# Optimization experiments

Measured on AMD Instinct MI355X. Metric: run time of the kernel, lower is better.

The kernel has to match this reference:

```python
import jax, jax.numpy as jnp
import numpy as np

U, H = 1024, 4096  # num_users, hidden_size; d_inner = 2*H = 8192


def setup_inputs() -> dict:
    key = jax.random.key(0)
    k0, k1, k2, k3 = jax.random.split(key, 4)
    x = jax.random.normal(k0, (U, H), dtype=jnp.float32)
    ssm_proj = jax.random.uniform(k1, (H, 2 * H), dtype=jnp.float32)  # torch.rand init
    conv_states = jnp.zeros((4, U, 2 * H), dtype=jnp.float32)          # ttnn.zeros init
    conv_wts = jax.random.uniform(k2, (4, 2 * H), dtype=jnp.float32)   # 4 taps, per-channel
    conv_bias = jax.random.uniform(k3, (2 * H,), dtype=jnp.float32)
    return {"x": x, "ssm_proj": ssm_proj, "conv_states": conv_states,
            "conv_wts": conv_wts, "conv_bias": conv_bias}


def reference(x, ssm_proj, conv_states, conv_wts, conv_bias):
    # in-projection: [U,H] @ [H,2H] -> [U,2H]
    xp = x @ ssm_proj
    # shift the 4-tap causal-conv state cache and append current step
    new_states = jnp.concatenate([conv_states[1:], xp[None]], axis=0)  # [4,U,2H]
    # depthwise 4-tap causal conv as weighted sum over taps + bias
    out = jnp.einsum("kd,kud->ud", conv_wts, new_states) + conv_bias   # [U,2H]
    # (downstream TtMambaSSM consumes `out`; external class, not part of this block's math)
    return out, new_states
```

## Files before the change

kernel.cpp:

```cpp
#include <hip/hip_runtime.h>
#include <hip/hip_bf16.h>

#define U_DIM 1024
#define H_DIM 4096
#define N_DIM 8192
#define K_DIM 4096

#define BM 128
#define BN 256
#define BK 64
#define NT (K_DIM / BK)
#define SLOTB (BM*BK*2 + BN*BK*2)

typedef __attribute__((ext_vector_type(8))) short bf16x8;
typedef __attribute__((ext_vector_type(4))) float f32x4;

__device__ inline unsigned short f2bf(float f) {
  union { float f; unsigned u; } a; a.f = f;
  unsigned r = a.u + 0x7fffu + ((a.u >> 16) & 1u);
  return (unsigned short)(r >> 16);
}

__device__ inline void gload_lds16(const void* g, void* l) {
  __builtin_amdgcn_global_load_lds(
      (const __attribute__((address_space(1))) unsigned*)(g),
      (__attribute__((address_space(3))) unsigned*)(l), 16, 0, 0);
}

#define TRANS_BLOCKS ((N_DIM / 64) * (K_DIM / 64))
__global__ __launch_bounds__(256) void prep_kernel(
    const float* __restrict__ B, unsigned short* __restrict__ Bt,
    const float* __restrict__ x, unsigned short* __restrict__ xb) {
  const int tid = threadIdx.x;
  if (blockIdx.x >= TRANS_BLOCKS) {
    size_t i = (size_t)(blockIdx.x - TRANS_BLOCKS) * 256 + tid;
    float4 v = ((const float4*)x)[i];
    ushort4 o;
    o.x = f2bf(v.x); o.y = f2bf(v.y); o.z = f2bf(v.z); o.w = f2bf(v.w);
    ((ushort4*)xb)[i] = o;
    return;
  }
  __shared__ float tile[64][65];
  const int kt = blockIdx.x & 63;
  const int nt = blockIdx.x >> 6;
  const int k0 = kt * 64, n0 = nt * 64;
  const int lr = tid >> 4;
  const int lc = (tid & 15) * 4;
#pragma unroll
  for (int it = 0; it < 4; ++it) {
    int r = it * 16 + lr;
    float4 v = *(const float4*)(&B[(size_t)(k0 + r) * N_DIM + n0 + lc]);
    tile[r][lc + 0] = v.x; tile[r][lc + 1] = v.y;
    tile[r][lc + 2] = v.z; tile[r][lc + 3] = v.w;
  }
  __syncthreads();
  const int sc = tid & 7;
  const int sr = tid >> 3;
#pragma unroll
  for (int it = 0; it < 2; ++it) {
    int rn = it * 32 + sr;
    union { bf16x8 v; unsigned short u[8]; } o;
#pragma unroll
    for (int j = 0; j < 8; ++j) o.u[j] = f2bf(tile[sc * 8 + j][rn]);
    *(bf16x8*)(&Bt[(size_t)(n0 + rn) * K_DIM + k0 + sc * 8]) = o.v;
  }
}

template <bool FUSE>
__global__ __launch_bounds__(512, 1) void gemm_conv_kernel(
    const unsigned short* __restrict__ Abf,
    const unsigned short* __restrict__ Btbf,
    const float* __restrict__ conv_states,
    const float* __restrict__ conv_wts,
    const float* __restrict__ conv_bias,
    float* __restrict__ out,
    float* __restrict__ ns)
{
  __shared__ char smem[3 * SLOTB];

  const int orig = blockIdx.x;
  const int bid  = (orig & 7) * 32 + (orig >> 3);
  const int brow = bid & 7;
  const int bcol = bid >> 3;
  const int tid  = threadIdx.x;
  const int lane = tid & 63;
  const int wid  = tid >> 6;
  const int wr = wid >> 2;
  const int wc = wid & 3;

  f32x4 acc[4][4];
#pragma unroll
  for (int m = 0; m < 4; ++m)
#pragma unroll
    for (int n = 0; n < 4; ++n)
#pragma unroll
      for (int r = 0; r < 4; ++r) acc[m][n][r] = 0.0f;

  const int rowa = tid >> 3;
  const int gsl  = (tid & 7) ^ (rowa & 7);
  const int tid16 = tid * 16;
  const unsigned short* gA0 = Abf  + (size_t)(brow * BM + rowa) * K_DIM + gsl * 8;
  const unsigned short* gA1 = gA0 + (size_t)64 * K_DIM;
  const unsigned short* gB0 = Btbf + (size_t)(bcol * BN + rowa) * K_DIM + gsl * 8;
  const unsigned short* gB1 = gB0 + (size_t)64  * K_DIM;
  const unsigned short* gB2 = gB0 + (size_t)128 * K_DIM;
  const unsigned short* gB3 = gB0 + (size_t)192 * K_DIM;

#define STAGE(kt, base) do {                               \
    const size_t ko = (size_t)(kt) * BK;                   \
    gload_lds16(gA0 + ko, (base) + tid16);                 \
    gload_lds16(gA1 + ko, (base) + 8192  + tid16);         \
    gload_lds16(gB0 + ko, (base) + 16384 + tid16);         \
    gload_lds16(gB1 + ko, (base) + 24576 + tid16);         \
    gload_lds16(gB2 + ko, (base) + 32768 + tid16);         \
    gload_lds16(gB3 + ko, (base) + 40960 + tid16);         \
  } while (0)

  const int l15 = lane & 15;
  const int fs  = lane >> 4;
  const int rsw = l15 & 7;
  int aoff[4], boff[4];
#pragma unroll
  for (int m = 0; m < 4; ++m) aoff[m] = (wr * 64 + m * 16 + l15) * 128;
#pragma unroll
  for (int n = 0; n < 4; ++n) boff[n] = (wc * 64 + n * 16 + l15) * 128;

  STAGE(0, smem);
  STAGE(1, smem + SLOTB);
  asm volatile("s_waitcnt vmcnt(6)" ::: "memory");
  __builtin_amdgcn_s_barrier();
  __builtin_amdgcn_sched_barrier(0);

  int s0 = 0, s2 = 2;
#pragma unroll 1
  for (int t = 0; t < NT; ++t) {
    if (t + 2 < NT) STAGE(t + 2, smem + s2 * SLOTB);

    const char* curA = smem + s0 * SLOTB;
    const char* curB = curA + 16384;
#pragma unroll
    for (int kh = 0; kh < 2; ++kh) {
      const int ksl = ((kh * 4 + fs) ^ rsw) * 16;
      bf16x8 af[4], bv[4];
#pragma unroll
      for (int m = 0; m < 4; ++m) af[m] = *(const bf16x8*)(curA + aoff[m] + ksl);
#pragma unroll
      for (int n = 0; n < 4; ++n) bv[n] = *(const bf16x8*)(curB + boff[n] + ksl);
      __builtin_amdgcn_s_setprio(1);
#pragma unroll
      for (int m = 0; m < 4; ++m)
#pragma unroll
        for (int n = 0; n < 4; ++n)
          acc[m][n] = __builtin_amdgcn_mfma_f32_16x16x32_bf16(af[m], bv[n], acc[m][n], 0, 0, 0);
      __builtin_amdgcn_s_setprio(0);
    }

    if (t + 2 < NT) asm volatile("s_waitcnt vmcnt(6) lgkmcnt(0)" ::: "memory");
    else            asm volatile("s_waitcnt vmcnt(0) lgkmcnt(0)" ::: "memory");
    __builtin_amdgcn_s_barrier();
    __builtin_amdgcn_sched_barrier(0);

    s0 = (s0 == 2) ? 0 : s0 + 1;
    s2 = (s2 == 2) ? 0 : s2 + 1;
  }
#undef STAGE

  float* cbuf = (float*)smem;
#pragma unroll
  for (int m = 0; m < 4; ++m)
#pragma unroll
    for (int n = 0; n < 4; ++n) {
      const int colb = (wc * 64 + n * 16 + l15) ^ (fs << 3);
#pragma unroll
      for (int r = 0; r < 4; ++r) {
        const int row = wr * 64 + m * 16 + fs * 4 + r;
        cbuf[row * 256 + colb] = acc[m][n][r];
      }
    }
  __syncthreads();

  const size_t PL4 = (size_t)U_DIM * (N_DIM / 4);
  const float4* cs1 = (const float4*)conv_states + PL4;
  const float4* cs2 = (const float4*)conv_states + 2 * PL4;
  const float4* cs3 = (const float4*)conv_states + 3 * PL4;
  float4* out4 = (float4*)out;
  float4* ns0 = (float4*)ns;
  float4* ns1 = ns0 + PL4;
  float4* ns2 = ns0 + 2 * PL4;
  float4* ns3 = ns0 + 3 * PL4;
  const float4* wt4 = (const float4*)conv_wts;
  const float4* bi4 = (const float4*)conv_bias;

#pragma unroll 1
  for (int i = 0; i < 16; ++i) {
    const int g    = i * 512 + tid;
    const int lrow = g >> 6;
    const int d4   = g & 63;
    const int fsr  = (lrow >> 2) & 3;
    const float4 xp4 = *(const float4*)&cbuf[lrow * 256 + ((d4 * 4) ^ (fsr << 3))];

    const int u = brow * BM + lrow;
    const int dcol4 = bcol * (BN / 4) + d4;
    const size_t gf4 = (size_t)u * (N_DIM / 4) + dcol4;

    const float4 w0 = wt4[dcol4];
    const float4 w1 = wt4[(N_DIM / 4) + dcol4];
    const float4 w2 = wt4[2 * (N_DIM / 4) + dcol4];
    const float4 w3 = wt4[3 * (N_DIM / 4) + dcol4];
    const float4 bs = bi4[dcol4];
    const float4 c1 = cs1[gf4];
    const float4 c2 = cs2[gf4];
    const float4 c3 = cs3[gf4];

    float4 o;
    o.x = fmaf(w0.x, c1.x, fmaf(w1.x, c2.x, fmaf(w2.x, c3.x, fmaf(w3.x, xp4.x, bs.x))));
    o.y = fmaf(w0.y, c1.y, fmaf(w1.y, c2.y, fmaf(w2.y, c3.y, fmaf(w3.y, xp4.y, bs.y))));
    o.z = fmaf(w0.z, c1.z, fmaf(w1.z, c2.z, fmaf(w2.z, c3.z, fmaf(w3.z, xp4.z, bs.z))));
    o.w = fmaf(w0.w, c1.w, fmaf(w1.w, c2.w, fmaf(w2.w, c3.w, fmaf(w3.w, xp4.w, bs.w))));

    out4[gf4] = o;
    if (FUSE) { ns0[gf4] = c1; ns1[gf4] = c2; ns2[gf4] = c3; }
    ns3[gf4] = xp4;
  }
}

extern "C" void kernel_launch(void* const* d_in, const int* in_sizes, int n_in,
                              void* d_out, int out_size, void* d_ws, size_t ws_size,
                              hipStream_t stream) {
  (void)in_sizes; (void)n_in; (void)out_size;
  const float* x           = (const float*)d_in[0];
  const float* ssm_proj    = (const float*)d_in[1];
  const float* conv_states = (const float*)d_in[2];
  const float* conv_wts    = (const float*)d_in[3];
  const float* conv_bias   = (const float*)d_in[4];
  float* outp = (float*)d_out;

  const size_t OUT_ELEMS = (size_t)U_DIM * N_DIM;
  float* ns = outp + OUT_ELEMS;

  const size_t BT_BYTES = (size_t)N_DIM * K_DIM * sizeof(unsigned short);
  const size_t XB_BYTES = (size_t)U_DIM * K_DIM * sizeof(unsigned short);
  const int GRID = (U_DIM / BM) * (N_DIM / BN);
  const int PREP_GRID = TRANS_BLOCKS + (U_DIM * H_DIM / 4) / 256;

  if (ws_size >= BT_BYTES + XB_BYTES) {
    unsigned short* Btbf = (unsigned short*)d_ws;
    unsigned short* xbf  = (unsigned short*)((char*)d_ws + BT_BYTES);
    prep_kernel<<<PREP_GRID, 256, 0, stream>>>(ssm_proj, Btbf, x, xbf);
    gemm_conv_kernel<true><<<GRID, 512, 0, stream>>>(
        xbf, Btbf, conv_states, conv_wts, conv_bias, outp, ns);
  } else {
    unsigned short* Btbf = (unsigned short*)ns;
    unsigned short* xbf  = (unsigned short*)(ns + 2 * OUT_ELEMS);
    prep_kernel<<<PREP_GRID, 256, 0, stream>>>(ssm_proj, Btbf, x, xbf);
    gemm_conv_kernel<false><<<GRID, 512, 0, stream>>>(
        xbf, Btbf, conv_states, conv_wts, conv_bias, outp, ns);
    hipMemcpyAsync(ns, conv_states + OUT_ELEMS, 3 * OUT_ELEMS * sizeof(float),
                   hipMemcpyDeviceToDevice, stream);
  }
}
```

Baseline: 170.4 us.

## Shrink GEMM tiles to 128x128x32 and allow multiple blocks per CU

Reduces the block tile from 128x256 with BK 64 to 128x128 with BK 32. The per-thread staging, swizzle pattern, fragment offsets and epilogue indexing are rewritten to match the smaller tile. The launch bound now permits several resident blocks per CU, and the grid doubles to 512 blocks. The aim is better occupancy and CU load balance, so more waves hide memory latency. In exchange, each block gets less operand reuse, does fewer MFMAs per barrier, and the total global/L2 traffic for the B and A operands grows.

```diff
diff --git a/kernel.cpp b/kernel.cpp
--- a/kernel.cpp
+++ b/kernel.cpp
@@ -7,8 +7,8 @@
 #define K_DIM 4096
 
 #define BM 128
-#define BN 256
-#define BK 64
+#define BN 128
+#define BK 32
 #define NT (K_DIM / BK)
 #define SLOTB (BM*BK*2 + BN*BK*2)
 
@@ -67,7 +67,7 @@
 }
 
 template <bool FUSE>
-__global__ __launch_bounds__(512, 1) void gemm_conv_kernel(
+__global__ __launch_bounds__(512, 4) void gemm_conv_kernel(
     const unsigned short* __restrict__ Abf,
     const unsigned short* __restrict__ Btbf,
     const float* __restrict__ conv_states,
@@ -76,10 +76,10 @@
     float* __restrict__ out,
     float* __restrict__ ns)
 {
-  __shared__ char smem[3 * SLOTB];
+  __shared__ char smem[65536];
 
   const int orig = blockIdx.x;
-  const int bid  = (orig & 7) * 32 + (orig >> 3);
+  const int bid  = (orig & 7) * 64 + (orig >> 3);
   const int brow = bid & 7;
   const int bcol = bid >> 3;
   const int tid  = threadIdx.x;
@@ -88,46 +88,38 @@
   const int wr = wid >> 2;
   const int wc = wid & 3;
 
-  f32x4 acc[4][4];
+  f32x4 acc[4][2];
 #pragma unroll
   for (int m = 0; m < 4; ++m)
 #pragma unroll
-    for (int n = 0; n < 4; ++n)
+    for (int n = 0; n < 2; ++n)
 #pragma unroll
       for (int r = 0; r < 4; ++r) acc[m][n][r] = 0.0f;
 
-  const int rowa = tid >> 3;
-  const int gsl  = (tid & 7) ^ (rowa & 7);
-  const int tid16 = tid * 16;
-  const unsigned short* gA0 = Abf  + (size_t)(brow * BM + rowa) * K_DIM + gsl * 8;
-  const unsigned short* gA1 = gA0 + (size_t)64 * K_DIM;
-  const unsigned short* gB0 = Btbf + (size_t)(bcol * BN + rowa) * K_DIM + gsl * 8;
-  const unsigned short* gB1 = gB0 + (size_t)64  * K_DIM;
-  const unsigned short* gB2 = gB0 + (size_t)128 * K_DIM;
-  const unsigned short* gB3 = gB0 + (size_t)192 * K_DIM;
+  const int srow   = tid >> 2;
+  const int swslot = (tid & 3) ^ ((srow >> 1) & 3);
+  const int tid16  = tid * 16;
+  const unsigned short* gA0 = Abf  + (size_t)(brow * BM + srow) * K_DIM + swslot * 8;
+  const unsigned short* gB0 = Btbf + (size_t)(bcol * BN + srow) * K_DIM + swslot * 8;
 
 #define STAGE(kt, base) do {                               \
     const size_t ko = (size_t)(kt) * BK;                   \
     gload_lds16(gA0 + ko, (base) + tid16);                 \
-    gload_lds16(gA1 + ko, (base) + 8192  + tid16);         \
-    gload_lds16(gB0 + ko, (base) + 16384 + tid16);         \
-    gload_lds16(gB1 + ko, (base) + 24576 + tid16);         \
-    gload_lds16(gB2 + ko, (base) + 32768 + tid16);         \
-    gload_lds16(gB3 + ko, (base) + 40960 + tid16);         \
+    gload_lds16(gB0 + ko, (base) + 8192 + tid16);          \
   } while (0)
 
   const int l15 = lane & 15;
   const int fs  = lane >> 4;
-  const int rsw = l15 & 7;
-  int aoff[4], boff[4];
-#pragma unroll
-  for (int m = 0; m < 4; ++m) aoff[m] = (wr * 64 + m * 16 + l15) * 128;
-#pragma unroll
-  for (int n = 0; n < 4; ++n) boff[n] = (wc * 64 + n * 16 + l15) * 128;
+  const int rds = (fs ^ ((l15 >> 1) & 3)) * 16;
+  int aoff[4], boff[2];
+#pragma unroll
+  for (int m = 0; m < 4; ++m) aoff[m] = (wr * 64 + m * 16 + l15) * 64 + rds;
+#pragma unroll
+  for (int n = 0; n < 2; ++n) boff[n] = (wc * 32 + n * 16 + l15) * 64 + rds;
 
   STAGE(0, smem);
   STAGE(1, smem + SLOTB);
-  asm volatile("s_waitcnt vmcnt(6)" ::: "memory");
+  asm volatile("s_waitcnt vmcnt(2)" ::: "memory");
   __builtin_amdgcn_s_barrier();
   __builtin_amdgcn_sched_barrier(0);
 
@@ -136,27 +128,23 @@
   for (int t = 0; t < NT; ++t) {
     if (t + 2 < NT) STAGE(t + 2, smem + s2 * SLOTB);
 
-    const char* curA = smem + s0 * SLOTB;
-    const char* curB = curA + 16384;
-#pragma unroll
-    for (int kh = 0; kh < 2; ++kh) {
-      const int ksl = ((kh * 4 + fs) ^ rsw) * 16;
-      bf16x8 af[4], bv[4];
-#pragma unroll
-      for (int m = 0; m < 4; ++m) af[m] = *(const bf16x8*)(curA + aoff[m] + ksl);
-#pragma unroll
-      for (int n = 0; n < 4; ++n) bv[n] = *(const bf16x8*)(curB + boff[n] + ksl);
-      __builtin_amdgcn_s_setprio(1);
-#pragma unroll
-      for (int m = 0; m < 4; ++m)
-#pragma unroll
-        for (int n = 0; n < 4; ++n)
-          acc[m][n] = __builtin_amdgcn_mfma_f32_16x16x32_bf16(af[m], bv[n], acc[m][n], 0, 0, 0);
-      __builtin_amdgcn_s_setprio(0);
-    }
-
-    if (t + 2 < NT) asm volatile("s_waitcnt vmcnt(6) lgkmcnt(0)" ::: "memory");
-    else            asm volatile("s_waitcnt vmcnt(0) lgkmcnt(0)" ::: "memory");
+    const char* sA = smem + s0 * SLOTB;
+    const char* sB = sA + 8192;
+    bf16x8 af[4], bv[2];
+#pragma unroll
+    for (int m = 0; m < 4; ++m) af[m] = *(const bf16x8*)(sA + aoff[m]);
+#pragma unroll
+    for (int n = 0; n < 2; ++n) bv[n] = *(const bf16x8*)(sB + boff[n]);
+    __builtin_amdgcn_s_setprio(1);
+#pragma unroll
+    for (int m = 0; m < 4; ++m)
+#pragma unroll
+      for (int n = 0; n < 2; ++n)
+        acc[m][n] = __builtin_amdgcn_mfma_f32_16x16x32_bf16(af[m], bv[n], acc[m][n], 0, 0, 0);
+    __builtin_amdgcn_s_setprio(0);
+
+    if (t + 2 < NT)      asm volatile("s_waitcnt vmcnt(2) lgkmcnt(0)" ::: "memory");
+    else                 asm volatile("s_waitcnt vmcnt(0) lgkmcnt(0)" ::: "memory");
     __builtin_amdgcn_s_barrier();
     __builtin_amdgcn_sched_barrier(0);
 
@@ -169,12 +157,12 @@
 #pragma unroll
   for (int m = 0; m < 4; ++m)
 #pragma unroll
-    for (int n = 0; n < 4; ++n) {
-      const int colb = (wc * 64 + n * 16 + l15) ^ (fs << 3);
+    for (int n = 0; n < 2; ++n) {
+      const int colb = (wc * 32 + n * 16 + l15) ^ (fs << 3);
 #pragma unroll
       for (int r = 0; r < 4; ++r) {
         const int row = wr * 64 + m * 16 + fs * 4 + r;
-        cbuf[row * 256 + colb] = acc[m][n][r];
+        cbuf[row * 128 + colb] = acc[m][n][r];
       }
     }
   __syncthreads();
@@ -192,12 +180,12 @@
   const float4* bi4 = (const float4*)conv_bias;
 
 #pragma unroll 1
-  for (int i = 0; i < 16; ++i) {
+  for (int i = 0; i < 8; ++i) {
     const int g    = i * 512 + tid;
-    const int lrow = g >> 6;
-    const int d4   = g & 63;
+    const int lrow = g >> 5;
+    const int d4   = g & 31;
     const int fsr  = (lrow >> 2) & 3;
-    const float4 xp4 = *(const float4*)&cbuf[lrow * 256 + ((d4 * 4) ^ (fsr << 3))];
+    const float4 xp4 = *(const float4*)&cbuf[lrow * 128 + ((d4 * 4) ^ (fsr << 3))];
 
     const int u = brow * BM + lrow;
     const int dcol4 = bcol * (BN / 4) + d4;
```

Measured after the change: 188.3 us. +10.5%, slower.

## Add producer warps to overlap conv-state streaming with GEMM main loop

Applied to the files above, without the earlier changes.

Adds two extra warps per block (640 threads) that, during the GEMM k-loop, read the three old conv-state planes, compute the partial conv sum with bias, write it to the output, and copy the shifted states. The epilogue then only re-reads the partial output, adds the last-tap contribution from the GEMM result, and writes the new state plane. This hides the memory-bound conv traffic behind MFMA compute, at the cost of an extra read-modify-write of the output and more threads sharing the barrier. The x-to-bf16 conversion also now handles eight elements per thread.

```diff
diff --git a/kernel.cpp b/kernel.cpp
--- a/kernel.cpp
+++ b/kernel.cpp
@@ -28,16 +28,19 @@
 }
 
 #define TRANS_BLOCKS ((N_DIM / 64) * (K_DIM / 64))
+#define CONV_BLOCKS  ((U_DIM * H_DIM) / (256 * 8))
 __global__ __launch_bounds__(256) void prep_kernel(
     const float* __restrict__ B, unsigned short* __restrict__ Bt,
     const float* __restrict__ x, unsigned short* __restrict__ xb) {
   const int tid = threadIdx.x;
   if (blockIdx.x >= TRANS_BLOCKS) {
     size_t i = (size_t)(blockIdx.x - TRANS_BLOCKS) * 256 + tid;
-    float4 v = ((const float4*)x)[i];
-    ushort4 o;
-    o.x = f2bf(v.x); o.y = f2bf(v.y); o.z = f2bf(v.z); o.w = f2bf(v.w);
-    ((ushort4*)xb)[i] = o;
+    float4 v0 = ((const float4*)x)[2 * i];
+    float4 v1 = ((const float4*)x)[2 * i + 1];
+    union { bf16x8 v; unsigned short u[8]; } o;
+    o.u[0] = f2bf(v0.x); o.u[1] = f2bf(v0.y); o.u[2] = f2bf(v0.z); o.u[3] = f2bf(v0.w);
+    o.u[4] = f2bf(v1.x); o.u[5] = f2bf(v1.y); o.u[6] = f2bf(v1.z); o.u[7] = f2bf(v1.w);
+    ((bf16x8*)xb)[i] = o.v;
     return;
   }
   __shared__ float tile[64][65];
@@ -67,7 +70,7 @@
 }
 
 template <bool FUSE>
-__global__ __launch_bounds__(512, 1) void gemm_conv_kernel(
+__global__ __launch_bounds__(640, 1) void gemm_conv_kernel(
     const unsigned short* __restrict__ Abf,
     const unsigned short* __restrict__ Btbf,
     const float* __restrict__ conv_states,
@@ -85,7 +88,8 @@
   const int tid  = threadIdx.x;
   const int lane = tid & 63;
   const int wid  = tid >> 6;
-  const int wr = wid >> 2;
+  const bool is_compute = (wid < 8);
+  const int wr = (wid >> 2) & 1;
   const int wc = wid & 3;
 
   f32x4 acc[4][4];
@@ -96,9 +100,9 @@
 #pragma unroll
       for (int r = 0; r < 4; ++r) acc[m][n][r] = 0.0f;
 
-  const int rowa = tid >> 3;
+  const int rowa = (tid & 511) >> 3;
   const int gsl  = (tid & 7) ^ (rowa & 7);
-  const int tid16 = tid * 16;
+  const int tid16 = (tid & 511) * 16;
   const unsigned short* gA0 = Abf  + (size_t)(brow * BM + rowa) * K_DIM + gsl * 8;
   const unsigned short* gA1 = gA0 + (size_t)64 * K_DIM;
   const unsigned short* gB0 = Btbf + (size_t)(bcol * BN + rowa) * K_DIM + gsl * 8;
@@ -125,61 +129,8 @@
 #pragma unroll
   for (int n = 0; n < 4; ++n) boff[n] = (wc * 64 + n * 16 + l15) * 128;
 
-  STAGE(0, smem);
-  STAGE(1, smem + SLOTB);
-  asm volatile("s_waitcnt vmcnt(6)" ::: "memory");
-  __builtin_amdgcn_s_barrier();
-  __builtin_amdgcn_sched_barrier(0);
-
-  int s0 = 0, s2 = 2;
-#pragma unroll 1
-  for (int t = 0; t < NT; ++t) {
-    if (t + 2 < NT) STAGE(t + 2, smem + s2 * SLOTB);
-
-    const char* curA = smem + s0 * SLOTB;
-    const char* curB = curA + 16384;
-#pragma unroll
-    for (int kh = 0; kh < 2; ++kh) {
-      const int ksl = ((kh * 4 + fs) ^ rsw) * 16;
-      bf16x8 af[4], bv[4];
-#pragma unroll
-      for (int m = 0; m < 4; ++m) af[m] = *(const bf16x8*)(curA + aoff[m] + ksl);
-#pragma unroll
-      for (int n = 0; n < 4; ++n) bv[n] = *(const bf16x8*)(curB + boff[n] + ksl);
-      __builtin_amdgcn_s_setprio(1);
-#pragma unroll
-      for (int m = 0; m < 4; ++m)
-#pragma unroll
-        for (int n = 0; n < 4; ++n)
-          acc[m][n] = __builtin_amdgcn_mfma_f32_16x16x32_bf16(af[m], bv[n], acc[m][n], 0, 0, 0);
-      __builtin_amdgcn_s_setprio(0);
-    }
-
-    if (t + 2 < NT) asm volatile("s_waitcnt vmcnt(6) lgkmcnt(0)" ::: "memory");
-    else            asm volatile("s_waitcnt vmcnt(0) lgkmcnt(0)" ::: "memory");
-    __builtin_amdgcn_s_barrier();
-    __builtin_amdgcn_sched_barrier(0);
-
-    s0 = (s0 == 2) ? 0 : s0 + 1;
-    s2 = (s2 == 2) ? 0 : s2 + 1;
-  }
-#undef STAGE
-
-  float* cbuf = (float*)smem;
-#pragma unroll
-  for (int m = 0; m < 4; ++m)
-#pragma unroll
-    for (int n = 0; n < 4; ++n) {
-      const int colb = (wc * 64 + n * 16 + l15) ^ (fs << 3);
-#pragma unroll
-      for (int r = 0; r < 4; ++r) {
-        const int row = wr * 64 + m * 16 + fs * 4 + r;
-        cbuf[row * 256 + colb] = acc[m][n][r];
-      }
-    }
-  __syncthreads();
-
   const size_t PL4 = (size_t)U_DIM * (N_DIM / 4);
+  const int    N4  = N_DIM / 4;
   const float4* cs1 = (const float4*)conv_states + PL4;
   const float4* cs2 = (const float4*)conv_states + 2 * PL4;
   const float4* cs3 = (const float4*)conv_states + 3 * PL4;
@@ -191,36 +142,103 @@
   const float4* wt4 = (const float4*)conv_wts;
   const float4* bi4 = (const float4*)conv_bias;
 
+  if (is_compute) {
+    STAGE(0, smem);
+    STAGE(1, smem + SLOTB);
+    asm volatile("s_waitcnt vmcnt(6)" ::: "memory");
+  }
+  __builtin_amdgcn_s_barrier();
+  __builtin_amdgcn_sched_barrier(0);
+
+  int s0 = 0, s2 = 2;
 #pragma unroll 1
-  for (int i = 0; i < 16; ++i) {
-    const int g    = i * 512 + tid;
-    const int lrow = g >> 6;
-    const int d4   = g & 63;
-    const int fsr  = (lrow >> 2) & 3;
-    const float4 xp4 = *(const float4*)&cbuf[lrow * 256 + ((d4 * 4) ^ (fsr << 3))];
-
-    const int u = brow * BM + lrow;
-    const int dcol4 = bcol * (BN / 4) + d4;
-    const size_t gf4 = (size_t)u * (N_DIM / 4) + dcol4;
-
-    const float4 w0 = wt4[dcol4];
-    const float4 w1 = wt4[(N_DIM / 4) + dcol4];
-    const float4 w2 = wt4[2 * (N_DIM / 4) + dcol4];
-    const float4 w3 = wt4[3 * (N_DIM / 4) + dcol4];
-    const float4 bs = bi4[dcol4];
-    const float4 c1 = cs1[gf4];
-    const float4 c2 = cs2[gf4];
-    const float4 c3 = cs3[gf4];
-
-    float4 o;
-    o.x = fmaf(w0.x, c1.x, fmaf(w1.x, c2.x, fmaf(w2.x, c3.x, fmaf(w3.x, xp4.x, bs.x))));
-    o.y = fmaf(w0.y, c1.y, fmaf(w1.y, c2.y, fmaf(w2.y, c3.y, fmaf(w3.y, xp4.y, bs.y))));
-    o.z = fmaf(w0.z, c1.z, fmaf(w1.z, c2.z, fmaf(w2.z, c3.z, fmaf(w3.z, xp4.z, bs.z))));
-    o.w = fmaf(w0.w, c1.w, fmaf(w1.w, c2.w, fmaf(w2.w, c3.w, fmaf(w3.w, xp4.w, bs.w))));
-
-    out4[gf4] = o;
-    if (FUSE) { ns0[gf4] = c1; ns1[gf4] = c2; ns2[gf4] = c3; }
-    ns3[gf4] = xp4;
+  for (int t = 0; t < NT; ++t) {
+    if (is_compute) {
+      if (t + 2 < NT) STAGE(t + 2, smem + s2 * SLOTB);
+
+      const char* curA = smem + s0 * SLOTB;
+      const char* curB = curA + 16384;
+#pragma unroll
+      for (int kh = 0; kh < 2; ++kh) {
+        const int ksl = ((kh * 4 + fs) ^ rsw) * 16;
+        bf16x8 af[4], bv[4];
+#pragma unroll
+        for (int m = 0; m < 4; ++m) af[m] = *(const bf16x8*)(curA + aoff[m] + ksl);
+#pragma unroll
+        for (int n = 0; n < 4; ++n) bv[n] = *(const bf16x8*)(curB + boff[n] + ksl);
+        __builtin_amdgcn_s_setprio(1);
+#pragma unroll
+        for (int m = 0; m < 4; ++m)
+#pragma unroll
+          for (int n = 0; n < 4; ++n)
+            acc[m][n] = __builtin_amdgcn_mfma_f32_16x16x32_bf16(af[m], bv[n], acc[m][n], 0, 0, 0);
+        __builtin_amdgcn_s_setprio(0);
+      }
+
+      if (t + 2 < NT) asm volatile("s_waitcnt vmcnt(6) lgkmcnt(0)" ::: "memory");
+      else            asm volatile("s_waitcnt vmcnt(0) lgkmcnt(0)" ::: "memory");
+    } else {
+      const int ctid = tid - 512;
+      const int g    = t * 128 + ctid;
+      const int lrow = g >> 6, d4 = g & 63;
+      const int dcol4 = bcol * N4 / 1 * 0 + bcol * (BN / 4) + d4;
+      const size_t gf4 = (size_t)(brow * BM + lrow) * N4 + dcol4;
+      const float4 c1 = cs1[gf4], c2 = cs2[gf4], c3 = cs3[gf4];
+      const float4 w0 = wt4[dcol4];
+      const float4 w1 = wt4[N4 + dcol4];
+      const float4 w2 = wt4[2 * N4 + dcol4];
+      const float4 bs = bi4[dcol4];
+      float4 pc;
+      pc.x = fmaf(w0.x, c1.x, fmaf(w1.x, c2.x, fmaf(w2.x, c3.x, bs.x)));
+      pc.y = fmaf(w0.y, c1.y, fmaf(w1.y, c2.y, fmaf(w2.y, c3.y, bs.y)));
+      pc.z = fmaf(w0.z, c1.z, fmaf(w1.z, c2.z, fmaf(w2.z, c3.z, bs.z)));
+      pc.w = fmaf(w0.w, c1.w, fmaf(w1.w, c2.w, fmaf(w2.w, c3.w, bs.w)));
+      out4[gf4] = pc;
+      if (FUSE) { ns0[gf4] = c1; ns1[gf4] = c2; ns2[gf4] = c3; }
+    }
+    __builtin_amdgcn_s_barrier();
+    __builtin_amdgcn_sched_barrier(0);
+
+    s0 = (s0 == 2) ? 0 : s0 + 1;
+    s2 = (s2 == 2) ? 0 : s2 + 1;
+  }
+#undef STAGE
+
+  float* cbuf = (float*)smem;
+  if (is_compute) {
+#pragma unroll
+    for (int m = 0; m < 4; ++m)
+#pragma unroll
+      for (int n = 0; n < 4; ++n) {
+        const int colb = (wc * 64 + n * 16 + l15) ^ (fs << 3);
+#pragma unroll
+        for (int r = 0; r < 4; ++r) {
+          const int row = wr * 64 + m * 16 + fs * 4 + r;
+          cbuf[row * 256 + colb] = acc[m][n][r];
+        }
+      }
+  }
+  __syncthreads();
+
+#pragma unroll 1
+  for (int p = 0; p < 13; ++p) {
+    const int g = p * 640 + tid;
+    if (g < 8192) {
+      const int lrow = g >> 6, d4 = g & 63;
+      const int fsr  = (lrow >> 2) & 3;
+      const float4 xp4 = *(const float4*)&cbuf[lrow * 256 + ((d4 * 4) ^ (fsr << 3))];
+      const int dcol4 = bcol * (BN / 4) + d4;
+      const size_t gf4 = (size_t)(brow * BM + lrow) * N4 + dcol4;
+      const float4 w3 = wt4[3 * N4 + dcol4];
+      const float4 pc = out4[gf4];
+      float4 o;
+      o.x = fmaf(w3.x, xp4.x, pc.x);
+      o.y = fmaf(w3.y, xp4.y, pc.y);
+      o.z = fmaf(w3.z, xp4.z, pc.z);
+      o.w = fmaf(w3.w, xp4.w, pc.w);
+      out4[gf4] = o;
+      ns3[gf4] = xp4;
+    }
   }
 }
 
@@ -241,19 +259,19 @@
   const size_t BT_BYTES = (size_t)N_DIM * K_DIM * sizeof(unsigned short);
   const size_t XB_BYTES = (size_t)U_DIM * K_DIM * sizeof(unsigned short);
   const int GRID = (U_DIM / BM) * (N_DIM / BN);
-  const int PREP_GRID = TRANS_BLOCKS + (U_DIM * H_DIM / 4) / 256;
+  const int PREP_GRID = TRANS_BLOCKS + CONV_BLOCKS;
 
   if (ws_size >= BT_BYTES + XB_BYTES) {
     unsigned short* Btbf = (unsigned short*)d_ws;
     unsigned short* xbf  = (unsigned short*)((char*)d_ws + BT_BYTES);
     prep_kernel<<<PREP_GRID, 256, 0, stream>>>(ssm_proj, Btbf, x, xbf);
-    gemm_conv_kernel<true><<<GRID, 512, 0, stream>>>(
+    gemm_conv_kernel<true><<<GRID, 640, 0, stream>>>(
         xbf, Btbf, conv_states, conv_wts, conv_bias, outp, ns);
   } else {
     unsigned short* Btbf = (unsigned short*)ns;
     unsigned short* xbf  = (unsigned short*)(ns + 2 * OUT_ELEMS);
     prep_kernel<<<PREP_GRID, 256, 0, stream>>>(ssm_proj, Btbf, x, xbf);
-    gemm_conv_kernel<false><<<GRID, 512, 0, stream>>>(
+    gemm_conv_kernel<false><<<GRID, 640, 0, stream>>>(
         xbf, Btbf, conv_states, conv_wts, conv_bias, outp, ns);
     hipMemcpyAsync(ns, conv_states + OUT_ELEMS, 3 * OUT_ELEMS * sizeof(float),
                    hipMemcpyDeviceToDevice, stream);
```

Result: slower. 187.3 us (+9.9%).
